# Performance work log

Hardware: AMD Instinct MI355X
Metric: run time of the kernel (lower is better)

The kernel has to match this reference:

```python
import jax, jax.numpy as jnp
import numpy as np

N = 100000   # nodes
E = 800000   # edges
IN = 128
H = 128
OUT = 64
EPS = 1e-5   # BatchNorm1d eps


def _bn(x, gamma, beta):
    # training-mode BatchNorm1d: batch mean / biased variance over nodes
    m = jnp.mean(x, axis=0)
    v = jnp.mean(jnp.square(x - m), axis=0)
    return (x - m) * jax.lax.rsqrt(v + EPS) * gamma + beta


def _sage_mean(h, src, dst, w_self, w_neigh, b):
    # DGL SAGEConv(aggregator='mean'): mean over in-neighbors, then combine
    msg = h[src]                                            # [E, H] gather
    agg = jax.ops.segment_sum(msg, dst, num_segments=N)     # [N, H] scatter-add
    deg = jax.ops.segment_sum(jnp.ones((E,), h.dtype), dst, num_segments=N)
    mean = agg / jnp.maximum(deg, 1.0)[:, None]             # zero-degree -> 0
    return jax.nn.relu(h @ w_self.T + mean @ w_neigh.T + b)


def setup_inputs() -> dict:
    key = jax.random.key(0)
    ks = jax.random.split(key, 18)
    p = lambda k, s: (jax.random.normal(k, s, jnp.float32) * 0.05)
    return {
        "h": jax.random.normal(ks[0], (N, IN), jnp.float32),
        "W1": p(ks[1], (H, IN)), "b1": jnp.zeros((H,), jnp.float32),
        "g1": jnp.ones((H,), jnp.float32), "bt1": jnp.zeros((H,), jnp.float32),
        "Ws1": p(ks[2], (H, H)), "Wn1": p(ks[3], (H, H)), "bs1": jnp.zeros((H,), jnp.float32),
        "W2": p(ks[4], (H, H)), "b2": jnp.zeros((H,), jnp.float32),
        "g2": jnp.ones((H,), jnp.float32), "bt2": jnp.zeros((H,), jnp.float32),
        "Ws2": p(ks[5], (H, H)), "Wn2": p(ks[6], (H, H)), "bs2": jnp.zeros((H,), jnp.float32),
        "W3": p(ks[7], (OUT, H)), "b3": jnp.zeros((OUT,), jnp.float32),
        "src": jax.random.randint(ks[8], (E,), 0, N, dtype=jnp.int32),
        "dst": jax.random.randint(ks[9], (E,), 0, N, dtype=jnp.int32),
    }


def reference(h, W1, b1, g1, bt1, Ws1, Wn1, bs1,
              W2, b2, g2, bt2, Ws2, Wn2, bs2, W3, b3, src, dst):
    x = jax.nn.relu(_bn(h @ W1.T + b1, g1, bt1))            # dense1+BN+ReLU (dropout=eval/identity)
    x = _sage_mean(x, src, dst, Ws1, Wn1, bs1)              # SAGEConv1 (relu inside)
    x = jax.nn.relu(_bn(x @ W2.T + b2, g2, bt2))            # dense2+BN+ReLU
    x = _sage_mean(x, src, dst, Ws2, Wn2, bs2)              # SAGEConv2
    return jax.nn.relu(x @ W3.T + b3)                       # [N, OUT]
```

## Files before the change

### kernel.cpp

```cpp
#include <hip/hip_runtime.h>
#include <hip/hip_bf16.h>
#include <cstddef>


#define NN 100000
#define NE 800000
#define EPB 2048
#define NBLK ((NE + EPB - 1) / EPB)
#define NBUK ((NN + 511) / 512)
#define CSRCAP (NE + NBUK * 1536)

typedef __attribute__((ext_vector_type(8))) short short8;
typedef __attribute__((ext_vector_type(4))) float f32x4;

__device__ inline unsigned short f2bf(float f) {
    unsigned int u = __float_as_uint(f);
    u += 0x7fff + ((u >> 16) & 1);
    return (unsigned short)(u >> 16);
}
__device__ inline float lo16f(unsigned u) { return __uint_as_float(u << 16); }
__device__ inline float hi16f(unsigned u) { return __uint_as_float(u & 0xffff0000u); }

#define GLOAD16(gp, lp)                                                              \
    __builtin_amdgcn_global_load_lds((const __attribute__((address_space(1))) unsigned int*)(gp), \
                                     (__attribute__((address_space(3))) unsigned int*)(lp), 16, 0, 0)


__global__ __launch_bounds__(256) void wcvt_kernel(const float* W1, const float* Ws1, const float* Wn1,
                                                   const float* W2, const float* Ws2, const float* Wn2,
                                                   const float* W3, unsigned short* out) {
    int g4 = blockIdx.x * 256 + threadIdx.x;
    if (g4 >= 26624) return;
    int e = g4 * 4;
    const float* src;
    int off;
    if (e < 98304) {
        int m = e >> 14;
        off = e & 16383;
        src = (m == 0) ? W1 : (m == 1) ? Ws1 : (m == 2) ? Wn1 : (m == 3) ? W2 : (m == 4) ? Ws2 : Wn2;
    } else {
        src = W3;
        off = e - 98304;
    }
    float4 v = *(const float4*)&src[off];
    ushort4 o = {f2bf(v.x), f2bf(v.y), f2bf(v.z), f2bf(v.w)};
    *(ushort4*)&out[e] = o;
}


__global__ __launch_bounds__(256) void hist_kernel(const int* __restrict__ dst, int* cnt, int E) {
    __shared__ int hh[NBUK];
    int t = threadIdx.x, blk = blockIdx.x;
    if (t < NBUK) hh[t] = 0;
    __syncthreads();
#pragma unroll
    for (int i = 0; i < EPB / 256; i++) {
        int e = blk * EPB + i * 256 + t;
        if (e < E) atomicAdd(&hh[dst[e] >> 9], 1);
    }
    __syncthreads();
    if (t < NBUK) cnt[t * NBLK + blk] = hh[t];
}

__global__ __launch_bounds__(512) void scan_blocks_kernel(int* cnt, int* btot) {
    __shared__ int s[512];
    int t = threadIdx.x, b = blockIdx.x;
    int v = (t < NBLK) ? cnt[b * NBLK + t] : 0;
    s[t] = v;
    __syncthreads();
#pragma unroll
    for (int off = 1; off < 512; off <<= 1) {
        int u = (t >= off) ? s[t - off] : 0;
        __syncthreads();
        s[t] += u;
        __syncthreads();
    }
    if (t < NBLK) cnt[b * NBLK + t] = s[t] - v;
    if (t == 511) btot[b] = s[511];
}

__global__ __launch_bounds__(256) void scan_buckets_kernel(const int* __restrict__ btot, int* bbase) {
    __shared__ int s[256];
    int t = threadIdx.x;
    int v = (t < NBUK) ? btot[t] : 0;
    s[t] = v;
    __syncthreads();
#pragma unroll
    for (int off = 1; off < 256; off <<= 1) {
        int u = (t >= off) ? s[t - off] : 0;
        __syncthreads();
        s[t] += u;
        __syncthreads();
    }
    if (t < NBUK) bbase[t] = s[t] - v;
}

__global__ __launch_bounds__(256) void scatter_kernel(const int* __restrict__ src,
                                                      const int* __restrict__ dst,
                                                      const int* __restrict__ cnt,
                                                      const int* __restrict__ bbase,
                                                      int* __restrict__ pairbuf, int E) {
    __shared__ int cur[NBUK];
    int t = threadIdx.x, blk = blockIdx.x;
    if (t < NBUK) cur[t] = cnt[t * NBLK + blk] + bbase[t];
    __syncthreads();
#pragma unroll
    for (int i = 0; i < EPB / 256; i++) {
        int e = blk * EPB + i * 256 + t;
        if (e < E) {
            int d = dst[e];
            int bk = d >> 9;
            int pos = atomicAdd(&cur[bk], 1);
            pairbuf[pos] = (src[e] << 9) | (d & 511);
        }
    }
}

__global__ __launch_bounds__(256) void fill_kernel(const int* __restrict__ pairbuf,
                                                   const int* __restrict__ bbase,
                                                   const int* __restrict__ btot,
                                                   int* __restrict__ row_ptr,
                                                   int* __restrict__ ideg,
                                                   int* __restrict__ csr_src, int n) {
    __shared__ int deg[512], pstart[512], cur[512], stmp[256];
    int t = threadIdx.x, b = blockIdx.x;
    int estart = bbase[b], ecnt = btot[b];
    int cbase = estart + b * 1536;
    deg[t] = 0;
    deg[t + 256] = 0;
    __syncthreads();
    for (int i = t; i < ecnt; i += 256) atomicAdd(&deg[pairbuf[estart + i] & 511], 1);
    __syncthreads();
    int d0 = deg[2 * t], d1 = deg[2 * t + 1];
    int p0 = (d0 + 3) & ~3, p1 = (d1 + 3) & ~3;
    int pair = p0 + p1;
    stmp[t] = pair;
    __syncthreads();
#pragma unroll
    for (int off = 1; off < 256; off <<= 1) {
        int u = (t >= off) ? stmp[t - off] : 0;
        __syncthreads();
        stmp[t] += u;
        __syncthreads();
    }
    int excl = stmp[t] - pair;
    pstart[2 * t] = excl;
    pstart[2 * t + 1] = excl + p0;
    cur[2 * t] = excl;
    cur[2 * t + 1] = excl + p0;
    int g = b * 512 + 2 * t;
    if (g < n) { row_ptr[g] = cbase + excl; ideg[g] = d0; }
    if (g + 1 < n) { row_ptr[g + 1] = cbase + excl + p0; ideg[g + 1] = d1; }
    __syncthreads();
    for (int i = t; i < ecnt; i += 256) {
        int v = pairbuf[estart + i];
        int p = atomicAdd(&cur[v & 511], 1);
        csr_src[cbase + p] = v >> 9;
    }
    __syncthreads();
#pragma unroll
    for (int l2 = 0; l2 < 2; l2++) {
        int l = t + l2 * 256;
        int d = deg[l], pd = (d + 3) & ~3;
        for (int j = d; j < pd; j++) csr_src[cbase + pstart[l] + j] = NN;
    }
}


__global__ __launch_bounds__(256) void gather_mean_kernel(const unsigned int* __restrict__ X32,
                                                          const int* __restrict__ row_ptr,
                                                          const int* __restrict__ ideg,
                                                          const int* __restrict__ csr_src,
                                                          unsigned int* __restrict__ Mout, int n) {
    int node = blockIdx.x * 4 + (threadIdx.x >> 6);
    if (node >= n) return;
    int lane = threadIdx.x & 63;
    int p = row_ptr[node];
    int deg = ideg[node];
    int pe = p + deg;
    float inv = 1.0f / fmaxf((float)deg, 1.0f);
    float a0 = 0.f, a1 = 0.f, b0 = 0.f, b1 = 0.f;
    for (int q = p; q < pe; q += 4) {
        int4 si = *(const int4*)&csr_src[q];
        unsigned u0 = X32[(size_t)si.x * 64 + lane];
        unsigned u1 = X32[(size_t)si.y * 64 + lane];
        unsigned u2 = X32[(size_t)si.z * 64 + lane];
        unsigned u3 = X32[(size_t)si.w * 64 + lane];
        a0 += lo16f(u0) + lo16f(u1);
        a1 += hi16f(u0) + hi16f(u1);
        b0 += lo16f(u2) + lo16f(u3);
        b1 += hi16f(u2) + hi16f(u3);
    }
    unsigned o = (unsigned)f2bf((a0 + b0) * inv) | ((unsigned)f2bf((a1 + b1) * inv) << 16);
    Mout[(size_t)node * 64 + lane] = o;
}


__global__ void bn_finalize_kernel(const float* __restrict__ stats, const float* __restrict__ gamma,
                                   const float* __restrict__ beta, float* bnp, float invM) {
    int c = threadIdx.x;
    float mean = stats[c] * invM;
    float var = stats[128 + c] * invM - mean * mean;
    float sc = gamma[c] * rsqrtf(var + 1e-5f);
    bnp[c] = sc;
    bnp[128 + c] = beta[c] - mean * sc;
}

__global__ __launch_bounds__(256) void bn_relu_kernel(const unsigned int* __restrict__ Yb,
                                                      const float* __restrict__ bnp,
                                                      unsigned int* __restrict__ X, int n8) {
    int gid = blockIdx.x * 256 + threadIdx.x;
    if (gid >= n8) return;
    int c0 = (gid & 15) * 8;
    float4 sA = *(const float4*)&bnp[c0];
    float4 sB = *(const float4*)&bnp[c0 + 4];
    float4 tA = *(const float4*)&bnp[128 + c0];
    float4 tB = *(const float4*)&bnp[128 + c0 + 4];
    uint4 u = ((const uint4*)Yb)[gid];
    uint4 o;
    o.x = (unsigned)f2bf(fmaxf(fmaf(lo16f(u.x), sA.x, tA.x), 0.f)) |
          ((unsigned)f2bf(fmaxf(fmaf(hi16f(u.x), sA.y, tA.y), 0.f)) << 16);
    o.y = (unsigned)f2bf(fmaxf(fmaf(lo16f(u.y), sA.z, tA.z), 0.f)) |
          ((unsigned)f2bf(fmaxf(fmaf(hi16f(u.y), sA.w, tA.w), 0.f)) << 16);
    o.z = (unsigned)f2bf(fmaxf(fmaf(lo16f(u.z), sB.x, tB.x), 0.f)) |
          ((unsigned)f2bf(fmaxf(fmaf(hi16f(u.z), sB.y, tB.y), 0.f)) << 16);
    o.w = (unsigned)f2bf(fmaxf(fmaf(lo16f(u.w), sB.z, tB.z), 0.f)) |
          ((unsigned)f2bf(fmaxf(fmaf(hi16f(u.w), sB.w, tB.w), 0.f)) << 16);
    ((uint4*)X)[gid] = o;
}


template <int NC, bool DUAL, bool RELU, bool STATS, bool OUTBF, bool BIAS, bool AF32>
__global__ __launch_bounds__(256) void gemm_hyb(const void* A1v, const unsigned short* __restrict__ W1b,
                                                const unsigned short* __restrict__ A2,
                                                const unsigned short* __restrict__ W2b,
                                                const float* __restrict__ bias, void* __restrict__ Cout,
                                                float* __restrict__ stats, int M) {
    constexpr int NG = NC / 16;
    constexpr int WBYTES = NC * 256;
    constexpr int NPASS = DUAL ? 2 : 1;
    __shared__ __align__(16) char smem[NPASS * WBYTES];

    const int tid = threadIdx.x;
    const int w = tid >> 6, lane = tid & 63;
    const int rl = lane & 15, kq = lane >> 4;
    const int m0 = blockIdx.x * 128;
    const int r0 = min(m0 + w * 32 + rl, M - 1);
    const int r1 = min(m0 + w * 32 + 16 + rl, M - 1);

#pragma unroll
    for (int p = 0; p < NPASS; p++) {
        const unsigned short* W = p ? W2b : W1b;
#pragma unroll
        for (int i = 0; i < NG; i++) {
            int iss = w * NG + i;
            int row = iss * 4 + (lane >> 4);
            int slot = (lane & 15) ^ (row & 7);
            GLOAD16((const char*)W + (size_t)row * 256 + (slot << 4),
                    smem + p * WBYTES + iss * 1024);
        }
    }
    __syncthreads();

    f32x4 acc[2][NG];
#pragma unroll
    for (int mt = 0; mt < 2; mt++)
#pragma unroll
        for (int g = 0; g < NG; g++) acc[mt][g] = (f32x4){0.f, 0.f, 0.f, 0.f};

#pragma unroll
    for (int pass = 0; pass < NPASS; ++pass) {
        const unsigned short* Ab = pass ? A2 : (const unsigned short*)A1v;
        const char* wbase = smem + pass * WBYTES;
#pragma unroll
        for (int ks = 0; ks < 4; ks++) {
            const int ko = ks * 32 + kq * 8;
            short8 a0, a1;
            if (AF32) {
                const float* Af = (const float*)A1v;
                float4 x0 = *(const float4*)&Af[(size_t)r0 * 128 + ko];
                float4 x1 = *(const float4*)&Af[(size_t)r0 * 128 + ko + 4];
                float4 y0 = *(const float4*)&Af[(size_t)r1 * 128 + ko];
                float4 y1 = *(const float4*)&Af[(size_t)r1 * 128 + ko + 4];
                a0 = (short8){(short)f2bf(x0.x), (short)f2bf(x0.y), (short)f2bf(x0.z), (short)f2bf(x0.w),
                              (short)f2bf(x1.x), (short)f2bf(x1.y), (short)f2bf(x1.z), (short)f2bf(x1.w)};
                a1 = (short8){(short)f2bf(y0.x), (short)f2bf(y0.y), (short)f2bf(y0.z), (short)f2bf(y0.w),
                              (short)f2bf(y1.x), (short)f2bf(y1.y), (short)f2bf(y1.z), (short)f2bf(y1.w)};
            } else {
                a0 = *(const short8*)&Ab[(size_t)r0 * 128 + ko];
                a1 = *(const short8*)&Ab[(size_t)r1 * 128 + ko];
            }
#pragma unroll
            for (int g = 0; g < NG; g++) {
                int wr = g * 16 + rl;
                short8 bw = *(const short8*)(wbase + wr * 256 + (((ks * 4 + kq) ^ (wr & 7)) << 4));
                acc[0][g] = __builtin_amdgcn_mfma_f32_16x16x32_bf16(a0, bw, acc[0][g], 0, 0, 0);
                acc[1][g] = __builtin_amdgcn_mfma_f32_16x16x32_bf16(a1, bw, acc[1][g], 0, 0, 0);
            }
        }
    }
    const int er = kq * 4;
#pragma unroll
    for (int mt = 0; mt < 2; mt++) {
        int rowb = m0 + w * 32 + mt * 16 + er;
#pragma unroll
        for (int g = 0; g < NG; g++) {
            int col = g * 16 + rl;
            float b = BIAS ? bias[col] : 0.f;
#pragma unroll
            for (int r = 0; r < 4; r++) {
                int row = rowb + r;
                if (row < M) {
                    float o = acc[mt][g][r] + b;
                    if (RELU) o = fmaxf(o, 0.f);
                    if (OUTBF)
                        ((unsigned short*)Cout)[(size_t)row * NC + col] = f2bf(o);
                    else
                        ((float*)Cout)[(size_t)row * NC + col] = o;
                }
            }
        }
    }
    if constexpr (STATS) {
        __syncthreads();
        float2* part = (float2*)smem;
        const int widx = w * 4 + kq;
#pragma unroll
        for (int g = 0; g < NG; g++) {
            float s = 0.f, q = 0.f;
#pragma unroll
            for (int mt = 0; mt < 2; mt++) {
                int rowb = m0 + w * 32 + mt * 16 + er;
#pragma unroll
                for (int r = 0; r < 4; r++)
                    if (rowb + r < M) {
                        float v = acc[mt][g][r];
                        s += v;
                        q += v * v;
                    }
            }
            part[widx * 128 + g * 16 + rl] = make_float2(s, q);
        }
        __syncthreads();
        if (tid < 128) {
            float s = 0.f, q = 0.f;
#pragma unroll
            for (int i = 0; i < 16; i++) {
                float2 v = part[i * 128 + tid];
                s += v.x;
                q += v.y;
            }
            atomicAdd(&stats[tid], s);
            atomicAdd(&stats[128 + tid], q);
        }
    }
}


extern "C" void kernel_launch(void* const* d_in, const int* in_sizes, int n_in,
                              void* d_out, int out_size, void* d_ws, size_t ws_size,
                              hipStream_t stream) {
    const float* h   = (const float*)d_in[0];
    const float* W1  = (const float*)d_in[1];
    const float* g1  = (const float*)d_in[3];
    const float* bt1 = (const float*)d_in[4];
    const float* Ws1 = (const float*)d_in[5];
    const float* Wn1 = (const float*)d_in[6];
    const float* bs1 = (const float*)d_in[7];
    const float* W2  = (const float*)d_in[8];
    const float* g2  = (const float*)d_in[10];
    const float* bt2 = (const float*)d_in[11];
    const float* Ws2 = (const float*)d_in[12];
    const float* Wn2 = (const float*)d_in[13];
    const float* bs2 = (const float*)d_in[14];
    const float* W3  = (const float*)d_in[15];
    const float* b3  = (const float*)d_in[16];
    const int* src   = (const int*)d_in[17];
    const int* dst   = (const int*)d_in[18];
    float* out = (float*)d_out;

    const int N = NN, E = NE;
    char* ws = (char*)d_ws;
    unsigned short* Xb = (unsigned short*)ws;
    unsigned short* Yb = (unsigned short*)(ws + 25600512);
    unsigned int* Mb = (unsigned int*)(ws + 51201024);
    char* tail = ws + 76801536;
    float* stats = (float*)tail;
    float* bnp = stats + 256;
    unsigned short* Wb = (unsigned short*)(bnp + 256);
    const unsigned short* Wb1  = Wb;
    const unsigned short* Wbs1 = Wb + 16384;
    const unsigned short* Wbn1 = Wb + 32768;
    const unsigned short* Wb2  = Wb + 49152;
    const unsigned short* Wbs2 = Wb + 65536;
    const unsigned short* Wbn2 = Wb + 81920;
    const unsigned short* Wb3  = Wb + 98304;

    int* ideg    = (int*)d_out;
    int* row_ptr = ideg + N;
    int* csr_src = row_ptr + N;
    int* pairbuf = csr_src + CSRCAP;
    int* cnt     = pairbuf + E;
    int* btot    = cnt + NBUK * NBLK;
    int* bbase   = btot + NBUK;

    const int gm = (N + 127) / 128;
    const int nw8 = (N * 16 + 255) / 256;
    const int gg = (N + 3) / 4;

    hipMemsetAsync(stats, 0, 256 * sizeof(float), stream);
    hipMemsetAsync(Xb + (size_t)N * 128, 0, 256, stream);
    wcvt_kernel<<<104, 256, 0, stream>>>(W1, Ws1, Wn1, W2, Ws2, Wn2, W3, Wb);
    hist_kernel<<<NBLK, 256, 0, stream>>>(dst, cnt, E);
    scan_blocks_kernel<<<NBUK, 512, 0, stream>>>(cnt, btot);
    scan_buckets_kernel<<<1, 256, 0, stream>>>(btot, bbase);
    scatter_kernel<<<NBLK, 256, 0, stream>>>(src, dst, cnt, bbase, pairbuf, E);
    fill_kernel<<<NBUK, 256, 0, stream>>>(pairbuf, bbase, btot, row_ptr, ideg, csr_src, N);

    gemm_hyb<128, false, false, true, true, false, true>
        <<<gm, 256, 0, stream>>>(h, Wb1, nullptr, nullptr, nullptr, Yb, stats, N);
    bn_finalize_kernel<<<1, 128, 0, stream>>>(stats, g1, bt1, bnp, 1.0f / N);
    bn_relu_kernel<<<nw8, 256, 0, stream>>>((const unsigned int*)Yb, bnp, (unsigned int*)Xb, N * 16);

    gather_mean_kernel<<<gg, 256, 0, stream>>>((const unsigned int*)Xb, row_ptr, ideg, csr_src, Mb, N);
    gemm_hyb<128, true, true, false, true, true, false>
        <<<gm, 256, 0, stream>>>(Xb, Wbs1, (const unsigned short*)Mb, Wbn1, bs1, Xb, nullptr, N);

    hipMemsetAsync(stats, 0, 256 * sizeof(float), stream);
    gemm_hyb<128, false, false, true, true, false, false>
        <<<gm, 256, 0, stream>>>(Xb, Wb2, nullptr, nullptr, nullptr, Yb, stats, N);
    bn_finalize_kernel<<<1, 128, 0, stream>>>(stats, g2, bt2, bnp, 1.0f / N);
    bn_relu_kernel<<<nw8, 256, 0, stream>>>((const unsigned int*)Yb, bnp, (unsigned int*)Xb, N * 16);

    gather_mean_kernel<<<gg, 256, 0, stream>>>((const unsigned int*)Xb, row_ptr, ideg, csr_src, Mb, N);
    gemm_hyb<128, true, true, false, true, true, false>
        <<<gm, 256, 0, stream>>>(Xb, Wbs2, (const unsigned short*)Mb, Wbn2, bs2, Xb, nullptr, N);

    gemm_hyb<64, false, true, false, false, true, false>
        <<<gm, 256, 0, stream>>>(Xb, Wb3, nullptr, nullptr, b3, out, nullptr, N);
}
```

Before: 280.5 us.

## Fold BN finalize into bn_relu, prescale CSR indices, halve GEMM LDS for dual pass

The separate bn_finalize launches go away: each bn_relu thread now recomputes the scale and shift from the raw stats. The two stats buffers are zeroed with a single memset, which removes a launch and a memset per layer. CSR source indices are stored premultiplied by 64 so the gather drops a 64-bit multiply per neighbour. The dual-pass GEMM now reuses one weight-sized LDS buffer, reloading weights between passes behind an extra barrier, and adds a launch_bounds occupancy hint of 4 blocks. In exchange each bn_relu thread does redundant rsqrt work, and the dual GEMM serialises the second weight load.

After: 276.2 us. Within noise of the previous version (-1.5%).

```diff
diff --git a/kernel.cpp b/kernel.cpp
--- a/kernel.cpp
+++ b/kernel.cpp
@@ -155,14 +155,14 @@
     for (int i = t; i < ecnt; i += 256) {
         int v = pairbuf[estart + i];
         int p = atomicAdd(&cur[v & 511], 1);
-        csr_src[cbase + p] = v >> 9;
+        csr_src[cbase + p] = (v >> 9) << 6;
     }
     __syncthreads();
 #pragma unroll
     for (int l2 = 0; l2 < 2; l2++) {
         int l = t + l2 * 256;
         int d = deg[l], pd = (d + 3) & ~3;
-        for (int j = d; j < pd; j++) csr_src[cbase + pstart[l] + j] = NN;
+        for (int j = d; j < pd; j++) csr_src[cbase + pstart[l] + j] = NN << 6;
     }
 }
 
@@ -182,10 +182,10 @@
     float a0 = 0.f, a1 = 0.f, b0 = 0.f, b1 = 0.f;
     for (int q = p; q < pe; q += 4) {
         int4 si = *(const int4*)&csr_src[q];
-        unsigned u0 = X32[(size_t)si.x * 64 + lane];
-        unsigned u1 = X32[(size_t)si.y * 64 + lane];
-        unsigned u2 = X32[(size_t)si.z * 64 + lane];
-        unsigned u3 = X32[(size_t)si.w * 64 + lane];
+        unsigned u0 = X32[si.x + lane];
+        unsigned u1 = X32[si.y + lane];
+        unsigned u2 = X32[si.z + lane];
+        unsigned u3 = X32[si.w + lane];
         a0 += lo16f(u0) + lo16f(u1);
         a1 += hi16f(u0) + hi16f(u1);
         b0 += lo16f(u2) + lo16f(u3);
@@ -196,50 +196,58 @@
 }
 
 
-__global__ void bn_finalize_kernel(const float* __restrict__ stats, const float* __restrict__ gamma,
-                                   const float* __restrict__ beta, float* bnp, float invM) {
-    int c = threadIdx.x;
-    float mean = stats[c] * invM;
-    float var = stats[128 + c] * invM - mean * mean;
-    float sc = gamma[c] * rsqrtf(var + 1e-5f);
-    bnp[c] = sc;
-    bnp[128 + c] = beta[c] - mean * sc;
-}
-
 __global__ __launch_bounds__(256) void bn_relu_kernel(const unsigned int* __restrict__ Yb,
-                                                      const float* __restrict__ bnp,
-                                                      unsigned int* __restrict__ X, int n8) {
+                                                      const float* __restrict__ stats,
+                                                      const float* __restrict__ gamma,
+                                                      const float* __restrict__ beta,
+                                                      unsigned int* __restrict__ X,
+                                                      float invN, int n8) {
     int gid = blockIdx.x * 256 + threadIdx.x;
     if (gid >= n8) return;
     int c0 = (gid & 15) * 8;
-    float4 sA = *(const float4*)&bnp[c0];
-    float4 sB = *(const float4*)&bnp[c0 + 4];
-    float4 tA = *(const float4*)&bnp[128 + c0];
-    float4 tB = *(const float4*)&bnp[128 + c0 + 4];
+    float4 s0 = *(const float4*)&stats[c0];
+    float4 s1 = *(const float4*)&stats[c0 + 4];
+    float4 q0 = *(const float4*)&stats[128 + c0];
+    float4 q1 = *(const float4*)&stats[128 + c0 + 4];
+    float4 g0 = *(const float4*)&gamma[c0];
+    float4 g1 = *(const float4*)&gamma[c0 + 4];
+    float4 b0 = *(const float4*)&beta[c0];
+    float4 b1 = *(const float4*)&beta[c0 + 4];
+    float sc[8], sh[8];
+    float m;
+    m = s0.x * invN; sc[0] = g0.x * rsqrtf(q0.x * invN - m * m + 1e-5f); sh[0] = b0.x - m * sc[0];
+    m = s0.y * invN; sc[1] = g0.y * rsqrtf(q0.y * invN - m * m + 1e-5f); sh[1] = b0.y - m * sc[1];
+    m = s0.z * invN; sc[2] = g0.z * rsqrtf(q0.z * invN - m * m + 1e-5f); sh[2] = b0.z - m * sc[2];
+    m = s0.w * invN; sc[3] = g0.w * rsqrtf(q0.w * invN - m * m + 1e-5f); sh[3] = b0.w - m * sc[3];
+    m = s1.x * invN; sc[4] = g1.x * rsqrtf(q1.x * invN - m * m + 1e-5f); sh[4] = b1.x - m * sc[4];
+    m = s1.y * invN; sc[5] = g1.y * rsqrtf(q1.y * invN - m * m + 1e-5f); sh[5] = b1.y - m * sc[5];
+    m = s1.z * invN; sc[6] = g1.z * rsqrtf(q1.z * invN - m * m + 1e-5f); sh[6] = b1.z - m * sc[6];
+    m = s1.w * invN; sc[7] = g1.w * rsqrtf(q1.w * invN - m * m + 1e-5f); sh[7] = b1.w - m * sc[7];
     uint4 u = ((const uint4*)Yb)[gid];
     uint4 o;
-    o.x = (unsigned)f2bf(fmaxf(fmaf(lo16f(u.x), sA.x, tA.x), 0.f)) |
-          ((unsigned)f2bf(fmaxf(fmaf(hi16f(u.x), sA.y, tA.y), 0.f)) << 16);
-    o.y = (unsigned)f2bf(fmaxf(fmaf(lo16f(u.y), sA.z, tA.z), 0.f)) |
-          ((unsigned)f2bf(fmaxf(fmaf(hi16f(u.y), sA.w, tA.w), 0.f)) << 16);
-    o.z = (unsigned)f2bf(fmaxf(fmaf(lo16f(u.z), sB.x, tB.x), 0.f)) |
-          ((unsigned)f2bf(fmaxf(fmaf(hi16f(u.z), sB.y, tB.y), 0.f)) << 16);
-    o.w = (unsigned)f2bf(fmaxf(fmaf(lo16f(u.w), sB.z, tB.z), 0.f)) |
-          ((unsigned)f2bf(fmaxf(fmaf(hi16f(u.w), sB.w, tB.w), 0.f)) << 16);
+    o.x = (unsigned)f2bf(fmaxf(fmaf(lo16f(u.x), sc[0], sh[0]), 0.f)) |
+          ((unsigned)f2bf(fmaxf(fmaf(hi16f(u.x), sc[1], sh[1]), 0.f)) << 16);
+    o.y = (unsigned)f2bf(fmaxf(fmaf(lo16f(u.y), sc[2], sh[2]), 0.f)) |
+          ((unsigned)f2bf(fmaxf(fmaf(hi16f(u.y), sc[3], sh[3]), 0.f)) << 16);
+    o.z = (unsigned)f2bf(fmaxf(fmaf(lo16f(u.z), sc[4], sh[4]), 0.f)) |
+          ((unsigned)f2bf(fmaxf(fmaf(hi16f(u.z), sc[5], sh[5]), 0.f)) << 16);
+    o.w = (unsigned)f2bf(fmaxf(fmaf(lo16f(u.w), sc[6], sh[6]), 0.f)) |
+          ((unsigned)f2bf(fmaxf(fmaf(hi16f(u.w), sc[7], sh[7]), 0.f)) << 16);
     ((uint4*)X)[gid] = o;
 }
 
 
 template <int NC, bool DUAL, bool RELU, bool STATS, bool OUTBF, bool BIAS, bool AF32>
-__global__ __launch_bounds__(256) void gemm_hyb(const void* A1v, const unsigned short* __restrict__ W1b,
-                                                const unsigned short* __restrict__ A2,
-                                                const unsigned short* __restrict__ W2b,
-                                                const float* __restrict__ bias, void* __restrict__ Cout,
-                                                float* __restrict__ stats, int M) {
+__global__ __launch_bounds__(256, 4) void gemm_hyb(const void* A1v,
+                                                   const unsigned short* __restrict__ W1b,
+                                                   const unsigned short* __restrict__ A2,
+                                                   const unsigned short* __restrict__ W2b,
+                                                   const float* __restrict__ bias,
+                                                   void* __restrict__ Cout,
+                                                   float* __restrict__ stats, int M) {
     constexpr int NG = NC / 16;
-    constexpr int WBYTES = NC * 256;
     constexpr int NPASS = DUAL ? 2 : 1;
-    __shared__ __align__(16) char smem[NPASS * WBYTES];
+    __shared__ __align__(16) char smem[NC * 256];
 
     const int tid = threadIdx.x;
     const int w = tid >> 6, lane = tid & 63;
@@ -248,20 +256,6 @@
     const int r0 = min(m0 + w * 32 + rl, M - 1);
     const int r1 = min(m0 + w * 32 + 16 + rl, M - 1);
 
-#pragma unroll
-    for (int p = 0; p < NPASS; p++) {
-        const unsigned short* W = p ? W2b : W1b;
-#pragma unroll
-        for (int i = 0; i < NG; i++) {
-            int iss = w * NG + i;
-            int row = iss * 4 + (lane >> 4);
-            int slot = (lane & 15) ^ (row & 7);
-            GLOAD16((const char*)W + (size_t)row * 256 + (slot << 4),
-                    smem + p * WBYTES + iss * 1024);
-        }
-    }
-    __syncthreads();
-
     f32x4 acc[2][NG];
 #pragma unroll
     for (int mt = 0; mt < 2; mt++)
@@ -270,8 +264,19 @@
 
 #pragma unroll
     for (int pass = 0; pass < NPASS; ++pass) {
+        if (pass) __syncthreads();
+        {
+            const unsigned short* W = pass ? W2b : W1b;
+#pragma unroll
+            for (int i = 0; i < NG; i++) {
+                int iss = w * NG + i;
+                int row = iss * 4 + kq;
+                int slot = rl ^ (row & 7);
+                GLOAD16((const char*)W + (size_t)row * 256 + (slot << 4), smem + iss * 1024);
+            }
+        }
+        __syncthreads();
         const unsigned short* Ab = pass ? A2 : (const unsigned short*)A1v;
-        const char* wbase = smem + pass * WBYTES;
 #pragma unroll
         for (int ks = 0; ks < 4; ks++) {
             const int ko = ks * 32 + kq * 8;
@@ -293,7 +298,7 @@
 #pragma unroll
             for (int g = 0; g < NG; g++) {
                 int wr = g * 16 + rl;
-                short8 bw = *(const short8*)(wbase + wr * 256 + (((ks * 4 + kq) ^ (wr & 7)) << 4));
+                short8 bw = *(const short8*)(smem + wr * 256 + (((ks * 4 + kq) ^ (wr & 7)) << 4));
                 acc[0][g] = __builtin_amdgcn_mfma_f32_16x16x32_bf16(a0, bw, acc[0][g], 0, 0, 0);
                 acc[1][g] = __builtin_amdgcn_mfma_f32_16x16x32_bf16(a1, bw, acc[1][g], 0, 0, 0);
             }
@@ -385,9 +390,9 @@
     unsigned short* Yb = (unsigned short*)(ws + 25600512);
     unsigned int* Mb = (unsigned int*)(ws + 51201024);
     char* tail = ws + 76801536;
-    float* stats = (float*)tail;
-    float* bnp = stats + 256;
-    unsigned short* Wb = (unsigned short*)(bnp + 256);
+    float* stats1 = (float*)tail;
+    float* stats2 = stats1 + 256;
+    unsigned short* Wb = (unsigned short*)(stats2 + 256);
     const unsigned short* Wb1  = Wb;
     const unsigned short* Wbs1 = Wb + 16384;
     const unsigned short* Wbn1 = Wb + 32768;
@@ -407,8 +412,9 @@
     const int gm = (N + 127) / 128;
     const int nw8 = (N * 16 + 255) / 256;
     const int gg = (N + 3) / 4;
-
-    hipMemsetAsync(stats, 0, 256 * sizeof(float), stream);
+    const float invN = 1.0f / N;
+
+    hipMemsetAsync(stats1, 0, 512 * sizeof(float), stream);
     hipMemsetAsync(Xb + (size_t)N * 128, 0, 256, stream);
     wcvt_kernel<<<104, 256, 0, stream>>>(W1, Ws1, Wn1, W2, Ws2, Wn2, W3, Wb);
     hist_kernel<<<NBLK, 256, 0, stream>>>(dst, cnt, E);
@@ -418,19 +424,18 @@
     fill_kernel<<<NBUK, 256, 0, stream>>>(pairbuf, bbase, btot, row_ptr, ideg, csr_src, N);
 
     gemm_hyb<128, false, false, true, true, false, true>
-        <<<gm, 256, 0, stream>>>(h, Wb1, nullptr, nullptr, nullptr, Yb, stats, N);
-    bn_finalize_kernel<<<1, 128, 0, stream>>>(stats, g1, bt1, bnp, 1.0f / N);
-    bn_relu_kernel<<<nw8, 256, 0, stream>>>((const unsigned int*)Yb, bnp, (unsigned int*)Xb, N * 16);
+        <<<gm, 256, 0, stream>>>(h, Wb1, nullptr, nullptr, nullptr, Yb, stats1, N);
+    bn_relu_kernel<<<nw8, 256, 0, stream>>>((const unsigned int*)Yb, stats1, g1, bt1,
+                                            (unsigned int*)Xb, invN, N * 16);
 
     gather_mean_kernel<<<gg, 256, 0, stream>>>((const unsigned int*)Xb, row_ptr, ideg, csr_src, Mb, N);
     gemm_hyb<128, true, true, false, true, true, false>
         <<<gm, 256, 0, stream>>>(Xb, Wbs1, (const unsigned short*)Mb, Wbn1, bs1, Xb, nullptr, N);
 
-    hipMemsetAsync(stats, 0, 256 * sizeof(float), stream);
     gemm_hyb<128, false, false, true, true, false, false>
-        <<<gm, 256, 0, stream>>>(Xb, Wb2, nullptr, nullptr, nullptr, Yb, stats, N);
-    bn_finalize_kernel<<<1, 128, 0, stream>>>(stats, g2, bt2, bnp, 1.0f / N);
-    bn_relu_kernel<<<nw8, 256, 0, stream>>>((const unsigned int*)Yb, bnp, (unsigned int*)Xb, N * 16);
+        <<<gm, 256, 0, stream>>>(Xb, Wb2, nullptr, nullptr, nullptr, Yb, stats2, N);
+    bn_relu_kernel<<<nw8, 256, 0, stream>>>((const unsigned int*)Yb, stats2, g2, bt2,
+                                            (unsigned int*)Xb, invN, N * 16);
 
     gather_mean_kernel<<<gg, 256, 0, stream>>>((const unsigned int*)Xb, row_ptr, ideg, csr_src, Mb, N);
     gemm_hyb<128, true, true, false, true, true, false>
```
